# Performance work log

Measured on AMD Instinct MI355X. Metric: run time of the kernel, lower is better.

The kernel has to match this reference:

```python
import jax, jax.numpy as jnp
import numpy as np
import math

N_EMBD = 768
N_HEAD = 12


def setup_inputs() -> dict:
    key = jax.random.key(0)
    k1, k2, k3, k4, k5 = jax.random.split(key, 5)
    B, T, C = 2, 4096, N_EMBD
    s_in = 1.0 / math.sqrt(C)
    x = jax.random.normal(k1, (B, T, C), dtype=jnp.float32)
    W_attn = jax.random.normal(k2, (C, 3 * C), dtype=jnp.float32) * s_in
    b_attn = jax.random.normal(k3, (3 * C,), dtype=jnp.float32) * 0.01
    W_proj = jax.random.normal(k4, (C, C), dtype=jnp.float32) * s_in
    b_proj = jax.random.normal(k5, (C,), dtype=jnp.float32) * 0.01
    return {"x": x, "W_attn": W_attn, "b_attn": b_attn, "W_proj": W_proj, "b_proj": b_proj}


def reference(x, W_attn, b_attn, W_proj, b_proj):
    B, T, C = x.shape
    H = N_HEAD
    D = C // H  # head dim
    qkv = x @ W_attn + b_attn  # [B,T,3C]
    # NOTE: original splits as (k, q, v) in that order
    k, q, v = jnp.split(qkv, 3, axis=2)
    # [B,T,C] -> [B,H,T,D]
    k = k.reshape(B, T, H, D).transpose(0, 2, 1, 3)
    q = q.reshape(B, T, H, D).transpose(0, 2, 1, 3)
    v = v.reshape(B, T, H, D).transpose(0, 2, 1, 3)
    scale = 1.0 / math.sqrt(D)
    scores = jnp.einsum('bhqd,bhkd->bhqk', q, k) * scale  # [B,H,T,T]
    causal = jnp.tril(jnp.ones((T, T), dtype=bool))
    scores = jnp.where(causal, scores, jnp.float32(-jnp.inf))
    weights = jax.nn.softmax(scores, axis=-1)  # attn dropout p=0 (eval)
    out = jnp.einsum('bhqk,bhkd->bhqd', weights, v)  # [B,H,T,D]
    out = out.transpose(0, 2, 1, 3).reshape(B, T, C)
    out = out @ W_proj + b_proj  # resid dropout p=0 (eval)
    return out
```

## Files before the change

### kernel.cpp

```cpp
#include <hip/hip_runtime.h>


#define TSEQ 4096
#define NH   12
#define HD   64
#define CEMB 768

typedef __attribute__((ext_vector_type(8))) short s8v;
typedef __attribute__((ext_vector_type(4))) float f32x4;

__device__ __forceinline__ ushort f2bf(float f) {
  union { float f; unsigned u; } x; x.f = f;
  unsigned u = x.u;
  u += 0x7fffu + ((u >> 16) & 1);
  return (ushort)(u >> 16);
}

__device__ __forceinline__ void gload16(const void* gsrc, void* ldst) {
  __builtin_amdgcn_global_load_lds(
      (const __attribute__((address_space(1))) unsigned int*)gsrc,
      (__attribute__((address_space(3))) unsigned int*)ldst, 16, 0, 0);
}

__global__ void cvt_x_kernel(const float* __restrict__ x, ushort* __restrict__ xb, int n4) {
  int i = blockIdx.x * blockDim.x + threadIdx.x;
  const int stride = gridDim.x * blockDim.x;
  for (; i < n4; i += stride) {
    float4 v = ((const float4*)x)[i];
    ushort4 o;
    o.x = f2bf(v.x); o.y = f2bf(v.y); o.z = f2bf(v.z); o.w = f2bf(v.w);
    ((ushort4*)xb)[i] = o;
  }
}

__global__ void transpose_cvt_kernel(const float* __restrict__ W, ushort* __restrict__ WT,
                                     int R, int Cn) {
  __shared__ ushort tile[32][33];
  const int bx = blockIdx.x * 32;
  const int by = blockIdx.y * 32;
  const int tx = threadIdx.x;
  const int ty = threadIdx.y;
#pragma unroll
  for (int i = ty; i < 32; i += 8)
    tile[i][tx] = f2bf(W[(size_t)(by + i) * Cn + bx + tx]);
  __syncthreads();
#pragma unroll
  for (int i = ty; i < 32; i += 8)
    WT[(size_t)(bx + i) * R + by + tx] = tile[tx][i];
}

__global__ void vtrans_kernel(const ushort* __restrict__ v, ushort* __restrict__ vT) {
  __shared__ ushort tile[64][65];
  const int bh = blockIdx.y;
  const int t0 = blockIdx.x * 64;
  const int tid = threadIdx.x;
  const int c = tid & 63, rg = tid >> 6;
  const ushort* vp = v + ((size_t)bh * TSEQ + t0) * HD;
#pragma unroll
  for (int i = 0; i < 16; ++i) {
    int row = rg * 16 + i;
    tile[row][c] = vp[(size_t)row * HD + c];
  }
  __syncthreads();
  ushort* op = vT + (size_t)bh * HD * TSEQ + t0;
#pragma unroll
  for (int i = 0; i < 16; ++i) {
    int d = rg * 16 + i;
    op[(size_t)d * TSEQ + c] = tile[c][d];
  }
}

#define QSC 0.18033688011112042f

template <int EPI>
__global__ void gemm128_kernel(const ushort* __restrict__ A, const ushort* __restrict__ Bt,
                               const float* __restrict__ bias,
                               ushort* __restrict__ oq, ushort* __restrict__ ok,
                               ushort* __restrict__ ov, float* __restrict__ fout,
                               int Ktot) {
  __shared__ ushort lA[128 * 32];
  __shared__ ushort lB[128 * 32];
  const int tid = threadIdx.x;
  const int bm = blockIdx.x, bn = blockIdx.y;
  const int wid = tid >> 6, lane = tid & 63;
  const int wr = wid >> 1, wc = wid & 1;
  const int lr = lane & 15, hi = lane >> 4;

  const f32x4 fzero = {0.f, 0.f, 0.f, 0.f};
  f32x4 acc[4][4];
#pragma unroll
  for (int m = 0; m < 4; ++m)
#pragma unroll
    for (int n = 0; n < 4; ++n) acc[m][n] = fzero;

  const int g0 = tid, g1 = tid + 256;
  const int rA0 = bm * 128 + (g0 >> 2), kO0 = (g0 & 3) * 8;
  const int rA1 = bm * 128 + (g1 >> 2), kO1 = (g1 & 3) * 8;
  const int rB0 = bn * 128 + (g0 >> 2);
  const int rB1 = bn * 128 + (g1 >> 2);

  for (int kt = 0; kt < Ktot; kt += 32) {
    __syncthreads();
    gload16(A + (size_t)rA0 * Ktot + kt + kO0, &lA[g0 * 8]);
    gload16(A + (size_t)rA1 * Ktot + kt + kO1, &lA[g1 * 8]);
    gload16(Bt + (size_t)rB0 * Ktot + kt + kO0, &lB[g0 * 8]);
    gload16(Bt + (size_t)rB1 * Ktot + kt + kO1, &lB[g1 * 8]);
    __syncthreads();
    s8v av[4], bv[4];
#pragma unroll
    for (int m = 0; m < 4; ++m)
      av[m] = *(const s8v*)&lA[(wr * 64 + m * 16 + lr) * 32 + hi * 8];
#pragma unroll
    for (int n = 0; n < 4; ++n)
      bv[n] = *(const s8v*)&lB[(wc * 64 + n * 16 + lr) * 32 + hi * 8];
#pragma unroll
    for (int m = 0; m < 4; ++m)
#pragma unroll
      for (int n = 0; n < 4; ++n)
        acc[m][n] = __builtin_amdgcn_mfma_f32_16x16x32_bf16(av[m], bv[n], acc[m][n], 0, 0, 0);
  }

  if (EPI == 0) {
    const int which = bn / 6;
#pragma unroll
    for (int n = 0; n < 4; ++n) {
      const int col = bn * 128 + wc * 64 + n * 16 + lr;
      const float bsv = bias[col];
      const int c = col - which * CEMB;
      const int h = c >> 6, d = c & 63;
#pragma unroll
      for (int m = 0; m < 4; ++m) {
        const int row0 = bm * 128 + wr * 64 + m * 16 + hi * 4;
#pragma unroll
        for (int r = 0; r < 4; ++r) {
          const int rgl = row0 + r;
          const int b = rgl >> 12, t = rgl & 4095;
          const float val = acc[m][n][r] + bsv;
          const size_t idx = ((size_t)(b * NH + h) * TSEQ + t) * HD + d;
          if (which == 0)      ok[idx] = f2bf(val);
          else if (which == 1) oq[idx] = f2bf(val * QSC);
          else                 ov[idx] = f2bf(val);
        }
      }
    }
  } else {
#pragma unroll
    for (int n = 0; n < 4; ++n) {
      const int col = bn * 128 + wc * 64 + n * 16 + lr;
      const float bsv = bias[col];
#pragma unroll
      for (int m = 0; m < 4; ++m) {
        const int row0 = bm * 128 + wr * 64 + m * 16 + hi * 4;
#pragma unroll
        for (int r = 0; r < 4; ++r)
          fout[(size_t)(row0 + r) * CEMB + col] = acc[m][n][r] + bsv;
      }
    }
  }
}

__global__ void attn_kernel(const ushort* __restrict__ qb, const ushort* __restrict__ kb,
                            const ushort* __restrict__ vT, ushort* __restrict__ ao) {
  __shared__ ushort lK[2][4096];
  __shared__ ushort lV[2][4096];
  __shared__ ushort lP[4][2048];

  const int bh = blockIdx.y;
  const int b = bh / NH, h = bh % NH;
  const int tid = threadIdx.x;
  const int wid = tid >> 6, lane = tid & 63;
  const int lr = lane & 15, hi = lane >> 4;
  const int qchunk = gridDim.x - 1 - blockIdx.x;
  const int wq = qchunk * 128 + wid * 32;

  const ushort* qpb = qb + ((size_t)bh * TSEQ) * HD;
  s8v qfr[2][2];
#pragma unroll
  for (int qf = 0; qf < 2; ++qf)
#pragma unroll
    for (int kh = 0; kh < 2; ++kh)
      qfr[qf][kh] = *(const s8v*)(qpb + (size_t)(wq + qf * 16 + lr) * HD + kh * 32 + hi * 8);

  const ushort* kpb = kb + (size_t)bh * TSEQ * HD;
  const ushort* vtb = vT + (size_t)bh * HD * TSEQ;

  const f32x4 fzero = {0.f, 0.f, 0.f, 0.f};
  f32x4 ot[4][2];
#pragma unroll
  for (int df = 0; df < 4; ++df)
#pragma unroll
    for (int qf = 0; qf < 2; ++qf) ot[df][qf] = fzero;
  float m_run[2] = {-1e30f, -1e30f};
  float l_run[2] = {0.f, 0.f};

  const int nt = qchunk * 2 + 2;
  const int sgc0 = wid * 64 + lane, sgc1 = sgc0 + 256;
  const int sr0 = sgc0 >> 3, sb0 = (sgc0 & 7) ^ (sr0 & 7);
  const int sr1 = sgc1 >> 3, sb1 = (sgc1 & 7) ^ (sr1 & 7);

#define STAGE(buf, kv0)                                               \
  do {                                                                \
    gload16(kpb + (size_t)((kv0) + sr0) * HD + sb0 * 8, &lK[buf][sgc0 * 8]); \
    gload16(vtb + (size_t)sr0 * TSEQ + (kv0) + sb0 * 8, &lV[buf][sgc0 * 8]); \
    gload16(kpb + (size_t)((kv0) + sr1) * HD + sb1 * 8, &lK[buf][sgc1 * 8]); \
    gload16(vtb + (size_t)sr1 * TSEQ + (kv0) + sb1 * 8, &lV[buf][sgc1 * 8]); \
  } while (0)

  STAGE(0, 0);
  asm volatile("s_waitcnt vmcnt(0)" ::: "memory");
  __syncthreads();

  int cur = 0;
  const int sw = (lr & 7) << 4;
  ushort* pw = lP[wid];

  for (int t = 0; t < nt; ++t) {
    const int kv0 = t * 64;
    if (t + 1 < nt) STAGE(cur ^ 1, kv0 + 64);

    if (kv0 <= wq + 31) {
      const char* lKb = (const char*)lK[cur];
      const char* lVb = (const char*)lV[cur];
      f32x4 st[4][2];
#pragma unroll
      for (int kvf = 0; kvf < 4; ++kvf) {
        const int row = kvf * 16 + lr;
        const s8v a0 = *(const s8v*)(lKb + row * 128 + ((hi * 16) ^ sw));
        const s8v a1 = *(const s8v*)(lKb + row * 128 + ((64 + hi * 16) ^ sw));
#pragma unroll
        for (int qf = 0; qf < 2; ++qf) {
          f32x4 s = fzero;
          s = __builtin_amdgcn_mfma_f32_16x16x32_bf16(a0, qfr[qf][0], s, 0, 0, 0);
          s = __builtin_amdgcn_mfma_f32_16x16x32_bf16(a1, qfr[qf][1], s, 0, 0, 0);
          st[kvf][qf] = s;
        }
      }

      if (kv0 + 63 > wq) {
#pragma unroll
        for (int kvf = 0; kvf < 4; ++kvf)
#pragma unroll
          for (int r = 0; r < 4; ++r) {
            const int kv = kv0 + kvf * 16 + hi * 4 + r;
#pragma unroll
            for (int qf = 0; qf < 2; ++qf)
              if (kv > wq + qf * 16 + lr) st[kvf][qf][r] = -1e30f;
          }
      }

#pragma unroll
      for (int qf = 0; qf < 2; ++qf) {
        float pmax = -1e30f;
#pragma unroll
        for (int kvf = 0; kvf < 4; ++kvf)
#pragma unroll
          for (int r = 0; r < 4; ++r) pmax = fmaxf(pmax, st[kvf][qf][r]);
        pmax = fmaxf(pmax, __shfl_xor(pmax, 16));
        pmax = fmaxf(pmax, __shfl_xor(pmax, 32));
        const float m_new = fmaxf(m_run[qf], pmax);
        const float sc = __builtin_amdgcn_exp2f(m_run[qf] - m_new);
        float psum = 0.f;
#pragma unroll
        for (int kvf = 0; kvf < 4; ++kvf)
#pragma unroll
          for (int r = 0; r < 4; ++r) {
            const float p = __builtin_amdgcn_exp2f(st[kvf][qf][r] - m_new);
            st[kvf][qf][r] = p;
            psum += p;
          }
        psum += __shfl_xor(psum, 16);
        psum += __shfl_xor(psum, 32);
        l_run[qf] = l_run[qf] * sc + psum;
        m_run[qf] = m_new;
#pragma unroll
        for (int df = 0; df < 4; ++df) {
          ot[df][qf][0] *= sc; ot[df][qf][1] *= sc;
          ot[df][qf][2] *= sc; ot[df][qf][3] *= sc;
        }
      }

#pragma unroll
      for (int qf = 0; qf < 2; ++qf) {
        const int rowb = (qf * 16 + lr) * 128;
#pragma unroll
        for (int kvf = 0; kvf < 4; ++kvf) {
          uint2 w;
          w.x = (uint)f2bf(st[kvf][qf][0]) | ((uint)f2bf(st[kvf][qf][1]) << 16);
          w.y = (uint)f2bf(st[kvf][qf][2]) | ((uint)f2bf(st[kvf][qf][3]) << 16);
          *(uint2*)((char*)pw + rowb + ((kvf * 32 + hi * 8) ^ sw)) = w;
        }
      }
      asm volatile("s_waitcnt lgkmcnt(0)" ::: "memory");
      __builtin_amdgcn_sched_barrier(0);

#pragma unroll
      for (int s = 0; s < 2; ++s) {
        s8v vf[4];
#pragma unroll
        for (int df = 0; df < 4; ++df) {
          const int row = df * 16 + lr;
          vf[df] = *(const s8v*)(lVb + row * 128 + ((s * 64 + hi * 16) ^ sw));
        }
#pragma unroll
        for (int qf = 0; qf < 2; ++qf) {
          const s8v pf = *(const s8v*)((char*)pw + (qf * 16 + lr) * 128 + ((s * 64 + hi * 16) ^ sw));
#pragma unroll
          for (int df = 0; df < 4; ++df)
            ot[df][qf] = __builtin_amdgcn_mfma_f32_16x16x32_bf16(vf[df], pf, ot[df][qf], 0, 0, 0);
        }
      }
    }

    asm volatile("s_waitcnt vmcnt(0)" ::: "memory");
    __syncthreads();
    cur ^= 1;
  }

#pragma unroll
  for (int qf = 0; qf < 2; ++qf) {
    const float inv_l = 1.f / l_run[qf];
    ushort* op = ao + ((size_t)(b * TSEQ + wq + qf * 16 + lr)) * CEMB + h * HD + hi * 4;
#pragma unroll
    for (int df = 0; df < 4; ++df) {
      ushort2 w0, w1;
      w0.x = f2bf(ot[df][qf][0] * inv_l); w0.y = f2bf(ot[df][qf][1] * inv_l);
      w1.x = f2bf(ot[df][qf][2] * inv_l); w1.y = f2bf(ot[df][qf][3] * inv_l);
      *(ushort2*)(op + df * 16) = w0;
      *(ushort2*)(op + df * 16 + 2) = w1;
    }
  }
#undef STAGE
}

extern "C" void kernel_launch(void* const* d_in, const int* in_sizes, int n_in,
                              void* d_out, int out_size, void* d_ws, size_t ws_size,
                              hipStream_t stream) {
  const float* x      = (const float*)d_in[0];
  const float* W_attn = (const float*)d_in[1];
  const float* b_attn = (const float*)d_in[2];
  const float* W_proj = (const float*)d_in[3];
  const float* b_proj = (const float*)d_in[4];
  float* out = (float*)d_out;

  char* ws = (char*)d_ws;
  ushort* xb  = (ushort*)(ws + 0);
  ushort* WaT = (ushort*)(ws + 12582912);
  ushort* WpT = (ushort*)(ws + 16121856);
  ushort* qbf = (ushort*)(ws + 17301504);
  ushort* kbf = (ushort*)(ws + 29884416);
  ushort* vbf = (ushort*)(ws + 42467328);
  ushort* vTb = (ushort*)(ws + 55050240);

  cvt_x_kernel<<<dim3(2048), dim3(256), 0, stream>>>(x, xb, (2 * TSEQ * CEMB) / 4);
  transpose_cvt_kernel<<<dim3(72, 24), dim3(32, 8), 0, stream>>>(W_attn, WaT, CEMB, 3 * CEMB);
  transpose_cvt_kernel<<<dim3(24, 24), dim3(32, 8), 0, stream>>>(W_proj, WpT, CEMB, CEMB);
  gemm128_kernel<0><<<dim3(64, 18), dim3(256), 0, stream>>>(xb, WaT, b_attn,
                                                            qbf, kbf, vbf, nullptr, CEMB);
  vtrans_kernel<<<dim3(64, 24), dim3(256), 0, stream>>>(vbf, vTb);
  attn_kernel<<<dim3(32, 24), dim3(256), 0, stream>>>(qbf, kbf, vTb, xb);
  gemm128_kernel<1><<<dim3(64, 6), dim3(256), 0, stream>>>(xb, WpT, b_proj,
                                                           nullptr, nullptr, nullptr, out, CEMB);
}
```

Measured before the change: 349.2 us.

## Pair mirrored causal query chunks per block for balanced attention work

Each attention block now handles two 64-row query chunks, one near the start and its mirror near the end of the sequence, so every block iterates 64-j KV tiles and the causal work is evened out across blocks. Each wave owns 16 rows from each chunk; the early chunk's QK and PV MFMAs and softmax are skipped once it is fully masked. The bf16 packing of probabilities also switches to the hardware v_cvt_pk_bf16_f32 instruction. This presumes the launch grid uses 32 blocks in x; the change adds branches and per-tile predication in exchange for load balance.

```diff
diff --git a/kernel.cpp b/kernel.cpp
--- a/kernel.cpp
+++ b/kernel.cpp
@@ -170,16 +170,17 @@
   const int tid = threadIdx.x;
   const int wid = tid >> 6, lane = tid & 63;
   const int lr = lane & 15, hi = lane >> 4;
-  const int qchunk = gridDim.x - 1 - blockIdx.x;
-  const int wq = qchunk * 128 + wid * 32;
+  const int j = blockIdx.x;
+  const int qmin0 = j * 64 + wid * 16;
+  const int qmin1 = (63 - j) * 64 + wid * 16;
 
   const ushort* qpb = qb + ((size_t)bh * TSEQ) * HD;
   s8v qfr[2][2];
 #pragma unroll
-  for (int qf = 0; qf < 2; ++qf)
-#pragma unroll
-    for (int kh = 0; kh < 2; ++kh)
-      qfr[qf][kh] = *(const s8v*)(qpb + (size_t)(wq + qf * 16 + lr) * HD + kh * 32 + hi * 8);
+  for (int kh = 0; kh < 2; ++kh) {
+    qfr[0][kh] = *(const s8v*)(qpb + (size_t)(qmin0 + lr) * HD + kh * 32 + hi * 8);
+    qfr[1][kh] = *(const s8v*)(qpb + (size_t)(qmin1 + lr) * HD + kh * 32 + hi * 8);
+  }
 
   const ushort* kpb = kb + (size_t)bh * TSEQ * HD;
   const ushort* vtb = vT + (size_t)bh * HD * TSEQ;
@@ -193,7 +194,7 @@
   float m_run[2] = {-1e30f, -1e30f};
   float l_run[2] = {0.f, 0.f};
 
-  const int nt = qchunk * 2 + 2;
+  const int nt = 64 - j;
   const int sgc0 = wid * 64 + lane, sgc1 = sgc0 + 256;
   const int sr0 = sgc0 >> 3, sb0 = (sgc0 & 7) ^ (sr0 & 7);
   const int sr1 = sgc1 >> 3, sb1 = (sgc1 & 7) ^ (sr1 & 7);
@@ -206,6 +207,49 @@
     gload16(vtb + (size_t)sr1 * TSEQ + (kv0) + sb1 * 8, &lV[buf][sgc1 * 8]); \
   } while (0)
 
+#define QFWORK(qf, QMIN)                                                     \
+  do {                                                                       \
+    if (kv0 + 63 > (QMIN)) {                                                 \
+      _Pragma("unroll") for (int kvf = 0; kvf < 4; ++kvf)                    \
+        _Pragma("unroll") for (int r = 0; r < 4; ++r)                        \
+          if (kv0 + kvf * 16 + hi * 4 + r > (QMIN) + lr)                     \
+            st[kvf][qf][r] = -1e30f;                                         \
+    }                                                                        \
+    float pmax = -1e30f;                                                     \
+    _Pragma("unroll") for (int kvf = 0; kvf < 4; ++kvf)                      \
+      _Pragma("unroll") for (int r = 0; r < 4; ++r)                          \
+        pmax = fmaxf(pmax, st[kvf][qf][r]);                                  \
+    pmax = fmaxf(pmax, __shfl_xor(pmax, 16));                                \
+    pmax = fmaxf(pmax, __shfl_xor(pmax, 32));                                \
+    const float m_new = fmaxf(m_run[qf], pmax);                              \
+    const float scq = __builtin_amdgcn_exp2f(m_run[qf] - m_new);             \
+    float psum = 0.f;                                                        \
+    _Pragma("unroll") for (int kvf = 0; kvf < 4; ++kvf)                      \
+      _Pragma("unroll") for (int r = 0; r < 4; ++r) {                        \
+        const float p = __builtin_amdgcn_exp2f(st[kvf][qf][r] - m_new);      \
+        st[kvf][qf][r] = p;                                                  \
+        psum += p;                                                           \
+      }                                                                      \
+    psum += __shfl_xor(psum, 16);                                            \
+    psum += __shfl_xor(psum, 32);                                            \
+    l_run[qf] = l_run[qf] * scq + psum;                                      \
+    m_run[qf] = m_new;                                                       \
+    _Pragma("unroll") for (int df = 0; df < 4; ++df) {                       \
+      ot[df][qf][0] *= scq; ot[df][qf][1] *= scq;                            \
+      ot[df][qf][2] *= scq; ot[df][qf][3] *= scq;                            \
+    }                                                                        \
+    const int rowb = ((qf) * 16 + lr) * 128;                                 \
+    _Pragma("unroll") for (int kvf = 0; kvf < 4; ++kvf) {                    \
+      uint wlo, whi;                                                         \
+      asm("v_cvt_pk_bf16_f32 %0, %1, %2"                                     \
+          : "=v"(wlo) : "v"(st[kvf][qf][0]), "v"(st[kvf][qf][1]));           \
+      asm("v_cvt_pk_bf16_f32 %0, %1, %2"                                     \
+          : "=v"(whi) : "v"(st[kvf][qf][2]), "v"(st[kvf][qf][3]));           \
+      uint2 w; w.x = wlo; w.y = whi;                                         \
+      *(uint2*)((char*)pw + rowb + ((kvf * 32 + hi * 8) ^ sw)) = w;          \
+    }                                                                        \
+  } while (0)
+
   STAGE(0, 0);
   asm volatile("s_waitcnt vmcnt(0)" ::: "memory");
   __syncthreads();
@@ -218,96 +262,53 @@
     const int kv0 = t * 64;
     if (t + 1 < nt) STAGE(cur ^ 1, kv0 + 64);
 
-    if (kv0 <= wq + 31) {
-      const char* lKb = (const char*)lK[cur];
-      const char* lVb = (const char*)lV[cur];
-      f32x4 st[4][2];
-#pragma unroll
-      for (int kvf = 0; kvf < 4; ++kvf) {
-        const int row = kvf * 16 + lr;
-        const s8v a0 = *(const s8v*)(lKb + row * 128 + ((hi * 16) ^ sw));
-        const s8v a1 = *(const s8v*)(lKb + row * 128 + ((64 + hi * 16) ^ sw));
-#pragma unroll
-        for (int qf = 0; qf < 2; ++qf) {
-          f32x4 s = fzero;
-          s = __builtin_amdgcn_mfma_f32_16x16x32_bf16(a0, qfr[qf][0], s, 0, 0, 0);
-          s = __builtin_amdgcn_mfma_f32_16x16x32_bf16(a1, qfr[qf][1], s, 0, 0, 0);
-          st[kvf][qf] = s;
-        }
-      }
-
-      if (kv0 + 63 > wq) {
-#pragma unroll
-        for (int kvf = 0; kvf < 4; ++kvf)
-#pragma unroll
-          for (int r = 0; r < 4; ++r) {
-            const int kv = kv0 + kvf * 16 + hi * 4 + r;
-#pragma unroll
-            for (int qf = 0; qf < 2; ++qf)
-              if (kv > wq + qf * 16 + lr) st[kvf][qf][r] = -1e30f;
-          }
-      }
-
-#pragma unroll
-      for (int qf = 0; qf < 2; ++qf) {
-        float pmax = -1e30f;
-#pragma unroll
-        for (int kvf = 0; kvf < 4; ++kvf)
-#pragma unroll
-          for (int r = 0; r < 4; ++r) pmax = fmaxf(pmax, st[kvf][qf][r]);
-        pmax = fmaxf(pmax, __shfl_xor(pmax, 16));
-        pmax = fmaxf(pmax, __shfl_xor(pmax, 32));
-        const float m_new = fmaxf(m_run[qf], pmax);
-        const float sc = __builtin_amdgcn_exp2f(m_run[qf] - m_new);
-        float psum = 0.f;
-#pragma unroll
-        for (int kvf = 0; kvf < 4; ++kvf)
-#pragma unroll
-          for (int r = 0; r < 4; ++r) {
-            const float p = __builtin_amdgcn_exp2f(st[kvf][qf][r] - m_new);
-            st[kvf][qf][r] = p;
-            psum += p;
-          }
-        psum += __shfl_xor(psum, 16);
-        psum += __shfl_xor(psum, 32);
-        l_run[qf] = l_run[qf] * sc + psum;
-        m_run[qf] = m_new;
-#pragma unroll
-        for (int df = 0; df < 4; ++df) {
-          ot[df][qf][0] *= sc; ot[df][qf][1] *= sc;
-          ot[df][qf][2] *= sc; ot[df][qf][3] *= sc;
-        }
-      }
-
-#pragma unroll
-      for (int qf = 0; qf < 2; ++qf) {
-        const int rowb = (qf * 16 + lr) * 128;
-#pragma unroll
-        for (int kvf = 0; kvf < 4; ++kvf) {
-          uint2 w;
-          w.x = (uint)f2bf(st[kvf][qf][0]) | ((uint)f2bf(st[kvf][qf][1]) << 16);
-          w.y = (uint)f2bf(st[kvf][qf][2]) | ((uint)f2bf(st[kvf][qf][3]) << 16);
-          *(uint2*)((char*)pw + rowb + ((kvf * 32 + hi * 8) ^ sw)) = w;
-        }
-      }
-      asm volatile("s_waitcnt lgkmcnt(0)" ::: "memory");
-      __builtin_amdgcn_sched_barrier(0);
-
-#pragma unroll
-      for (int s = 0; s < 2; ++s) {
-        s8v vf[4];
-#pragma unroll
-        for (int df = 0; df < 4; ++df) {
-          const int row = df * 16 + lr;
-          vf[df] = *(const s8v*)(lVb + row * 128 + ((s * 64 + hi * 16) ^ sw));
-        }
-#pragma unroll
-        for (int qf = 0; qf < 2; ++qf) {
-          const s8v pf = *(const s8v*)((char*)pw + (qf * 16 + lr) * 128 + ((s * 64 + hi * 16) ^ sw));
-#pragma unroll
-          for (int df = 0; df < 4; ++df)
-            ot[df][qf] = __builtin_amdgcn_mfma_f32_16x16x32_bf16(vf[df], pf, ot[df][qf], 0, 0, 0);
-        }
+    const char* lKb = (const char*)lK[cur];
+    const char* lVb = (const char*)lV[cur];
+    const bool act0 = (kv0 <= qmin0 + 15);
+
+    f32x4 st[4][2];
+#pragma unroll
+    for (int kvf = 0; kvf < 4; ++kvf) {
+      const int row = kvf * 16 + lr;
+      const s8v a0 = *(const s8v*)(lKb + row * 128 + ((hi * 16) ^ sw));
+      const s8v a1 = *(const s8v*)(lKb + row * 128 + ((64 + hi * 16) ^ sw));
+      f32x4 s1 = fzero;
+      s1 = __builtin_amdgcn_mfma_f32_16x16x32_bf16(a0, qfr[1][0], s1, 0, 0, 0);
+      s1 = __builtin_amdgcn_mfma_f32_16x16x32_bf16(a1, qfr[1][1], s1, 0, 0, 0);
+      st[kvf][1] = s1;
+      if (act0) {
+        f32x4 s0 = fzero;
+        s0 = __builtin_amdgcn_mfma_f32_16x16x32_bf16(a0, qfr[0][0], s0, 0, 0, 0);
+        s0 = __builtin_amdgcn_mfma_f32_16x16x32_bf16(a1, qfr[0][1], s0, 0, 0, 0);
+        st[kvf][0] = s0;
+      }
+    }
+
+    QFWORK(1, qmin1);
+    if (act0) QFWORK(0, qmin0);
+
+    asm volatile("s_waitcnt lgkmcnt(0)" ::: "memory");
+    __builtin_amdgcn_sched_barrier(0);
+
+#pragma unroll
+    for (int s = 0; s < 2; ++s) {
+      s8v vf[4];
+#pragma unroll
+      for (int df = 0; df < 4; ++df) {
+        const int row = df * 16 + lr;
+        vf[df] = *(const s8v*)(lVb + row * 128 + ((s * 64 + hi * 16) ^ sw));
+      }
+      {
+        const s8v pf = *(const s8v*)((char*)pw + (16 + lr) * 128 + ((s * 64 + hi * 16) ^ sw));
+#pragma unroll
+        for (int df = 0; df < 4; ++df)
+          ot[df][1] = __builtin_amdgcn_mfma_f32_16x16x32_bf16(vf[df], pf, ot[df][1], 0, 0, 0);
+      }
+      if (act0) {
+        const s8v pf = *(const s8v*)((char*)pw + lr * 128 + ((s * 64 + hi * 16) ^ sw));
+#pragma unroll
+        for (int df = 0; df < 4; ++df)
+          ot[df][0] = __builtin_amdgcn_mfma_f32_16x16x32_bf16(vf[df], pf, ot[df][0], 0, 0, 0);
       }
     }
 
@@ -318,8 +319,9 @@
 
 #pragma unroll
   for (int qf = 0; qf < 2; ++qf) {
+    const int qrow = (qf == 0 ? qmin0 : qmin1) + lr;
     const float inv_l = 1.f / l_run[qf];
-    ushort* op = ao + ((size_t)(b * TSEQ + wq + qf * 16 + lr)) * CEMB + h * HD + hi * 4;
+    ushort* op = ao + ((size_t)(b * TSEQ + qrow)) * CEMB + h * HD + hi * 4;
 #pragma unroll
     for (int df = 0; df < 4; ++df) {
       ushort2 w0, w1;
@@ -330,6 +332,7 @@
     }
   }
 #undef STAGE
+#undef QFWORK
 }
 
 extern "C" void kernel_launch(void* const* d_in, const int* in_sizes, int n_in,
```

After: 423.8 us. 1.21x slower.
